# Performance work log

Hardware: AMD Instinct MI355X
Metric: run time of the kernel (lower is better)

## Reference

```python
import jax, jax.numpy as jnp
import numpy as np

N_NODES = 50000
N_EDGES = 1600000
IN_DIM = 128
HID = 64
HEADS = 4
N_GRAPHS = 64
OUT_DIM = 10
NEG_SLOPE = 0.2  # PyG GATConv default leaky_relu slope


def _glorot(key, shape):
    fan_in = shape[0] if len(shape) > 1 else shape[-1]
    return jax.random.normal(key, shape, dtype=jnp.float32) / np.sqrt(fan_in)


def setup_inputs() -> dict:
    key = jax.random.key(0)
    ks = jax.random.split(key, 24)
    imgs = jax.random.normal(ks[0], (N_NODES, IN_DIM), dtype=jnp.float32)
    edge_index = jax.random.randint(ks[1], (2, N_EDGES), 0, N_NODES, dtype=jnp.int32)
    batch = jnp.sort(jax.random.randint(ks[2], (N_NODES,), 0, N_GRAPHS, dtype=jnp.int32))
    HC = HID * HEADS
    inp = {
        'imgs': imgs, 'edge_index': edge_index, 'batch': batch,
        # superpixel aggregator: Linear(input_dim, hidden)
        'W_agg': _glorot(ks[3], (IN_DIM, HID)), 'b_agg': jnp.zeros((HID,), jnp.float32),
        # GAT layer 0: hidden -> heads*hidden, concat
        'W0': _glorot(ks[4], (HID, HC)), 'as0': _glorot(ks[5], (HEADS, HID)), 'ad0': _glorot(ks[6], (HEADS, HID)), 'b0': jnp.zeros((HC,), jnp.float32),
        # GAT layer 1: heads*hidden -> heads*hidden, concat
        'W1': _glorot(ks[7], (HC, HC)), 'as1': _glorot(ks[8], (HEADS, HID)), 'ad1': _glorot(ks[9], (HEADS, HID)), 'b1': jnp.zeros((HC,), jnp.float32),
        # GAT layer 2: heads*hidden -> hidden, mean over heads
        'W2': _glorot(ks[10], (HC, HC)), 'as2': _glorot(ks[11], (HEADS, HID)), 'ad2': _glorot(ks[12], (HEADS, HID)), 'b2': jnp.zeros((HID,), jnp.float32),
        # MLP: hidden -> hidden -> out
        'mW1': _glorot(ks[13], (HID, HID)), 'mb1': jnp.zeros((HID,), jnp.float32),
        'mW2': _glorot(ks[14], (HID, OUT_DIM)), 'mb2': jnp.zeros((OUT_DIM,), jnp.float32),
    }
    return inp


def _gat_conv(x, src, dst, W, a_src, a_dst, b, concat):
    # PyG GATConv: linear -> per-head scores -> leaky_relu -> segment softmax over dst -> scatter-add
    N = x.shape[0]
    H, C = a_src.shape
    h = (x @ W).reshape(N, H, C)                      # [N,H,C]
    es = jnp.sum(h * a_src, axis=-1)                  # [N,H]
    ed = jnp.sum(h * a_dst, axis=-1)                  # [N,H]
    e = jax.nn.leaky_relu(es[src] + ed[dst], NEG_SLOPE)  # [E,H]
    m = jax.ops.segment_max(e, dst, num_segments=N)
    m = jnp.where(jnp.isfinite(m), m, 0.0)
    ex = jnp.exp(e - m[dst])                          # [E,H]
    s = jax.ops.segment_sum(ex, dst, num_segments=N)
    alpha = ex / (s[dst] + 1e-16)                     # [E,H]
    out = jax.ops.segment_sum(h[src] * alpha[..., None], dst, num_segments=N)  # [N,H,C]
    out = out.reshape(N, H * C) if concat else out.mean(axis=1)
    return out + b


def _forward(imgs, edge_index, batch, W_agg, b_agg, W0, as0, ad0, b0, W1, as1, ad1, b1, W2, as2, ad2, b2, mW1, mb1, mW2, mb2):
    N = imgs.shape[0]
    # add self loops (PyG GATConv default add_self_loops=True)
    loop = jnp.arange(N, dtype=edge_index.dtype)
    src = jnp.concatenate([edge_index[0], loop])
    dst = jnp.concatenate([edge_index[1], loop])
    x = imgs @ W_agg + b_agg                          # lrgb aggregator
    x = jax.nn.elu(_gat_conv(x, src, dst, W0, as0, ad0, b0, True))
    x = jax.nn.elu(_gat_conv(x, src, dst, W1, as1, ad1, b1, True))
    x = _gat_conv(x, src, dst, W2, as2, ad2, b2, False)
    # global mean pool over graphs
    sums = jax.ops.segment_sum(x, batch, num_segments=N_GRAPHS)
    cnt = jax.ops.segment_sum(jnp.ones((N,), x.dtype), batch, num_segments=N_GRAPHS)
    pooled = sums / jnp.maximum(cnt, 1.0)[:, None]
    # MLP (dropout inactive at inference)
    hmlp = jax.nn.relu(pooled @ mW1 + mb1)
    return hmlp @ mW2 + mb2


def reference(imgs, edge_index, batch, W_agg, b_agg, W0, as0, ad0, b0, W1, as1, ad1, b1, W2, as2, ad2, b2, mW1, mb1, mW2, mb2):
    return _forward(imgs, edge_index, batch, W_agg, b_agg, W0, as0, ad0, b0, W1, as1, ad1, b1, W2, as2, ad2, b2, mW1, mb1, mW2, mb2)
```

## Files before the change

### kernel.cpp

```cpp
#include <hip/hip_runtime.h>
#include <hip/hip_bf16.h>

#define N_NODES 50000
#define N_EDGESX 1600000
#define E_TOT   (N_EDGESX + N_NODES)
#define IN_DIM 128
#define HID 64
#define HEADS 4
#define HC 256
#define N_GRAPHS 64
#define OUT_DIM 10
#define NEG_SLOPE 0.2f

#define NBUK 196
#define CAP 12288
#define BT 4096

typedef __attribute__((ext_vector_type(8))) short bf16x8;
typedef __attribute__((ext_vector_type(4))) float f32x4;

__device__ __forceinline__ float lrelu(float x){ return fmaxf(x, NEG_SLOPE*x); }
__device__ __forceinline__ float sel4(float4 v, int i){
  float r = v.x;
  r = (i==1) ? v.y : r;
  r = (i==2) ? v.z : r;
  r = (i==3) ? v.w : r;
  return r;
}
__device__ __forceinline__ unsigned short f2bf(float f){
  union { __hip_bfloat16 b; unsigned short u; } cv;
  cv.b = __float2bfloat16(f);
  return cv.u;
}
__device__ __forceinline__ float bflo(unsigned int u){ return __uint_as_float(u << 16); }
__device__ __forceinline__ float bfhi(unsigned int u){ return __uint_as_float(u & 0xffff0000u); }

__global__ __launch_bounds__(256) void bin_k(const int* __restrict__ ei,
                                             int* __restrict__ bucket_cursor,
                                             unsigned int* __restrict__ bucket_buf){
  __shared__ unsigned int pk[BT];
  __shared__ unsigned int binned[BT];
  __shared__ int hist[256], excl[256], gbase[256], lcur[256], tmp[256];
  const int tid = threadIdx.x;
  const int e0 = blockIdx.x * BT;
  const int nv = min(BT, E_TOT - e0);
  hist[tid] = 0;
  __syncthreads();
  for (int i = tid; i < nv; i += 256){
    int e = e0 + i;
    int src, dst;
    if (e < N_EDGESX){ src = ei[e]; dst = ei[N_EDGESX + e]; }
    else { src = e - N_EDGESX; dst = src; }
    pk[i] = ((unsigned)src << 16) | (unsigned)dst;
    atomicAdd(&hist[dst >> 8], 1);
  }
  __syncthreads();
  int v = hist[tid];
  tmp[tid] = v;
  __syncthreads();
  for (int off = 1; off < 256; off <<= 1){
    int t = (tid >= off) ? tmp[tid-off] : 0;
    __syncthreads();
    tmp[tid] += t;
    __syncthreads();
  }
  excl[tid] = tmp[tid] - v;
  lcur[tid] = tmp[tid] - v;
  if (tid < NBUK && v > 0) gbase[tid] = atomicAdd(&bucket_cursor[tid], v);
  __syncthreads();
  for (int i = tid; i < nv; i += 256){
    unsigned u = pk[i];
    int b = (int)((u & 0xFFFFu) >> 8);
    int p = atomicAdd(&lcur[b], 1);
    binned[p] = u;
  }
  __syncthreads();
  for (int j = tid; j < nv; j += 256){
    unsigned u = binned[j];
    int b = (int)((u & 0xFFFFu) >> 8);
    bucket_buf[(size_t)b*CAP + gbase[b] + (j - excl[b])] = u;
  }
}

__global__ __launch_bounds__(256) void bucket_scan_k(const int* __restrict__ bucket_cursor,
                                                     int* __restrict__ bucket_base,
                                                     int* __restrict__ row_start){
  __shared__ int tmp[256];
  int t = threadIdx.x;
  int v = (t < NBUK) ? bucket_cursor[t] : 0;
  tmp[t] = v;
  __syncthreads();
  for (int off = 1; off < 256; off <<= 1){
    int x = (t >= off) ? tmp[t-off] : 0;
    __syncthreads();
    tmp[t] += x;
    __syncthreads();
  }
  if (t < NBUK) bucket_base[t] = tmp[t] - v;
  if (t == 0) row_start[N_NODES] = E_TOT;
}

__global__ __launch_bounds__(256) void build_k(const unsigned int* __restrict__ bucket_buf,
                                               const int* __restrict__ bucket_cursor,
                                               const int* __restrict__ bucket_base,
                                               int* __restrict__ row_start,
                                               int* __restrict__ csr_src){
  __shared__ int hist[256], excl[256], lcur[256], tmp[256];
  const int b = blockIdx.x;
  const int t = threadIdx.x;
  const int cntb = bucket_cursor[b];
  const int base = bucket_base[b];
  const unsigned int* buf = bucket_buf + (size_t)b*CAP;
  hist[t] = 0;
  __syncthreads();
  for (int i = t; i < cntb; i += 256) atomicAdd(&hist[buf[i] & 255], 1);
  __syncthreads();
  int v = hist[t];
  tmp[t] = v;
  __syncthreads();
  for (int off = 1; off < 256; off <<= 1){
    int x = (t >= off) ? tmp[t-off] : 0;
    __syncthreads();
    tmp[t] += x;
    __syncthreads();
  }
  excl[t] = tmp[t] - v;
  lcur[t] = tmp[t] - v;
  int g = b*256 + t;
  if (g < N_NODES) row_start[g] = base + excl[t];
  __syncthreads();
  for (int i = t; i < cntb; i += 256){
    unsigned u = buf[i];
    int p = atomicAdd(&lcur[u & 255], 1);
    csr_src[base + p] = (int)(u >> 16);
  }
}

__global__ __launch_bounds__(256) void wcvt_k(const float* __restrict__ W, unsigned short* __restrict__ WT, int K){
  int idx = blockIdx.x*256 + threadIdx.x;
  if (idx >= K*256) return;
  int k = idx >> 8, c = idx & 255;
  WT[c*K + k] = f2bf(W[k*256 + c]);
}

__global__ __launch_bounds__(256) void wproj_k(const float* __restrict__ W0,
    const float* __restrict__ as0, const float* __restrict__ ad0,
    float* __restrict__ ws0, float* __restrict__ wd0){
  int t = threadIdx.x;
  int h = t >> 6, k = t & 63;
  float s = 0.f, d = 0.f;
  for (int c = 0; c < 64; c++){
    float wv = W0[k*256 + h*64 + c];
    s = fmaf(wv, as0[h*64 + c], s);
    d = fmaf(wv, ad0[h*64 + c], d);
  }
  ws0[t] = s; wd0[t] = d;
}

__global__ __launch_bounds__(256) void agg_lin(const float* __restrict__ imgs, const float* __restrict__ W,
                                               const float* __restrict__ b,
                                               const float* __restrict__ ws0, const float* __restrict__ wd0,
                                               unsigned short* __restrict__ x0,
                                               float* __restrict__ es, float* __restrict__ ed){
  __shared__ __align__(16) float xr[4][IN_DIM];
  int w = threadIdx.x >> 6, lane = threadIdx.x & 63;
  int n = blockIdx.x*4 + w;
  if (n >= N_NODES) return;
  ((float2*)xr[w])[lane] = ((const float2*)(imgs + (size_t)n*IN_DIM))[lane];
  float acc = b[lane];
  #pragma unroll 8
  for (int k = 0; k < IN_DIM; k++)
    acc = fmaf(xr[w][k], W[k*HID + lane], acc);
  x0[(size_t)n*HID + lane] = f2bf(acc);
  float p[4], q[4];
  #pragma unroll
  for (int h = 0; h < 4; h++){
    p[h] = acc * ws0[h*64 + lane];
    q[h] = acc * wd0[h*64 + lane];
  }
  #pragma unroll
  for (int off = 32; off >= 1; off >>= 1){
    #pragma unroll
    for (int h = 0; h < 4; h++){
      p[h] += __shfl_xor(p[h], off);
      q[h] += __shfl_xor(q[h], off);
    }
  }
  if (lane == 0){
    float4 pv; pv.x=p[0]; pv.y=p[1]; pv.z=p[2]; pv.w=p[3];
    float4 qv; qv.x=q[0]; qv.y=q[1]; qv.z=q[2]; qv.w=q[3];
    *(float4*)(es + n*4) = pv;
    *(float4*)(ed + n*4) = qv;
  }
}

__global__ __launch_bounds__(256) void gat_agg0(const unsigned short* __restrict__ x0,
    const float* __restrict__ es, const float* __restrict__ ed,
    const int* __restrict__ row_start, const int* __restrict__ csr_src,
    unsigned short* __restrict__ y4){
  __shared__ int   sbuf[4][64];
  __shared__ float wbuf[4][64][4];
  const int lane = threadIdx.x & 63;
  const int wid  = threadIdx.x >> 6;
  const int n = blockIdx.x*4 + wid;
  if (n >= N_NODES) return;
  const int rs = row_start[n], re = row_start[n+1];
  const float4 edn = *(const float4*)(ed + n*4);
  const int slot = lane >> 3;
  const int f8   = lane & 7;
  float4 sumw = make_float4(0.f,0.f,0.f,0.f);
  float acc[4][8];
  #pragma unroll
  for (int h=0;h<4;h++)
    #pragma unroll
    for (int q2=0;q2<8;q2++) acc[h][q2]=0.f;

  for (int base = rs; base < re; base += 64){
    const int cl = min(64, re - base);
    int e = base + lane;
    int s = (e < re) ? csr_src[e] : 0;
    float4 e4 = *(const float4*)(es + (s<<2));
    float w0 = __expf(lrelu(e4.x + edn.x));
    float w1 = __expf(lrelu(e4.y + edn.y));
    float w2 = __expf(lrelu(e4.z + edn.z));
    float w3 = __expf(lrelu(e4.w + edn.w));
    if (e >= re){ w0=0.f; w1=0.f; w2=0.f; w3=0.f; }
    sumw.x += w0; sumw.y += w1; sumw.z += w2; sumw.w += w3;
    sbuf[wid][lane] = s;
    float4 wv; wv.x=w0; wv.y=w1; wv.z=w2; wv.w=w3;
    *(float4*)wbuf[wid][lane] = wv;
    for (int j = 0; j < cl; j += 8){
      int jj = j + slot;
      if (jj < cl){
        float4 aw = *(const float4*)wbuf[wid][jj];
        int s2 = sbuf[wid][jj];
        uint4 hv = *(const uint4*)(x0 + ((unsigned)(s2<<6) + (unsigned)(f8<<3)));
        float f[8] = {bflo(hv.x),bfhi(hv.x),bflo(hv.y),bfhi(hv.y),
                      bflo(hv.z),bfhi(hv.z),bflo(hv.w),bfhi(hv.w)};
        #pragma unroll
        for (int q2=0;q2<8;q2++){
          acc[0][q2] = fmaf(aw.x, f[q2], acc[0][q2]);
          acc[1][q2] = fmaf(aw.y, f[q2], acc[1][q2]);
          acc[2][q2] = fmaf(aw.z, f[q2], acc[2][q2]);
          acc[3][q2] = fmaf(aw.w, f[q2], acc[3][q2]);
        }
      }
    }
  }
  #pragma unroll
  for (int off = 8; off <= 32; off <<= 1){
    #pragma unroll
    for (int h=0;h<4;h++)
      #pragma unroll
      for (int q2=0;q2<8;q2++) acc[h][q2] += __shfl_xor(acc[h][q2], off);
  }
  #pragma unroll
  for (int off = 32; off >= 1; off >>= 1){
    sumw.x += __shfl_xor(sumw.x, off);
    sumw.y += __shfl_xor(sumw.y, off);
    sumw.z += __shfl_xor(sumw.z, off);
    sumw.w += __shfl_xor(sumw.w, off);
  }
  if (lane < 32){
    int h = lane >> 3;
    float inv = 1.f / (sel4(sumw, h) + 1e-16f);
    union { unsigned short u[8]; uint4 v; } ob;
    #pragma unroll
    for (int q2=0;q2<8;q2++) ob.u[q2] = f2bf(acc[h][q2] * inv);
    *(uint4*)(y4 + (size_t)n*HC + lane*8) = ob.v;
  }
}

__global__ __launch_bounds__(256) void hgemm_k(const unsigned short* __restrict__ y4,
                                               const unsigned short* __restrict__ WT0,
                                               const float* __restrict__ b0,
                                               unsigned short* __restrict__ x1){
  __shared__ __align__(16) unsigned short xs[16][264];
  const int tid = threadIdx.x;
  const int lane = tid & 63;
  const int w = tid >> 6;
  const int n0 = blockIdx.x * 16;
  for (int i = tid; i < 16*32; i += 256){
    int r = i >> 5, cc = (i & 31) * 8;
    *(uint4*)(&xs[r][cc]) = *(const uint4*)(y4 + (size_t)(n0+r)*HC + cc);
  }
  __syncthreads();
  const int g = lane >> 4, cl = lane & 15;
  f32x4 acc[4];
  #pragma unroll
  for (int c = 0; c < 4; c++) acc[c] = (f32x4){0.f,0.f,0.f,0.f};
  #pragma unroll
  for (int t = 0; t < 2; t++){
    bf16x8 a = *(const bf16x8*)(&xs[cl][w*64 + t*32 + g*8]);
    #pragma unroll
    for (int c = 0; c < 4; c++){
      bf16x8 bv = *(const bf16x8*)(WT0 + (size_t)(w*64 + c*16 + cl)*64 + t*32 + g*8);
      acc[c] = __builtin_amdgcn_mfma_f32_16x16x32_bf16(a, bv, acc[c], 0, 0, 0);
    }
  }
  #pragma unroll
  for (int c = 0; c < 4; c++){
    int col = w*64 + c*16 + cl;
    float bb = b0[col];
    #pragma unroll
    for (int j = 0; j < 4; j++){
      float v = acc[c][j] + bb;
      v = v > 0.f ? v : expm1f(v);
      x1[(size_t)(n0 + g*4 + j)*HC + col] = f2bf(v);
    }
  }
}

template<int K>
__global__ __launch_bounds__(256) void lin_mfma(const unsigned short* __restrict__ x,
                                                const unsigned short* __restrict__ WT,
                                                const float* __restrict__ as_, const float* __restrict__ ad_,
                                                unsigned short* __restrict__ h,
                                                float* __restrict__ es, float* __restrict__ ed){
  constexpr int KP = K + 8;
  __shared__ __align__(16) unsigned short xs[16][KP];
  const int tid = threadIdx.x;
  const int lane = tid & 63;
  const int w = tid >> 6;
  const int n0 = blockIdx.x * 16;
  constexpr int CH = K/8;
  for (int i = tid; i < 16*CH; i += 256){
    int r = i / CH, cc = (i % CH)*8;
    *(uint4*)(&xs[r][cc]) = *(const uint4*)(x + (size_t)(n0+r)*K + cc);
  }
  __syncthreads();
  const int g  = lane >> 4;
  const int cl = lane & 15;
  f32x4 acc[4];
  #pragma unroll
  for (int c = 0; c < 4; c++) acc[c] = (f32x4){0.f,0.f,0.f,0.f};
  #pragma unroll
  for (int t = 0; t < K/32; t++){
    bf16x8 a = *(const bf16x8*)(&xs[cl][t*32 + g*8]);
    #pragma unroll
    for (int c = 0; c < 4; c++){
      bf16x8 bv = *(const bf16x8*)(WT + (size_t)(w*64 + c*16 + cl)*K + t*32 + g*8);
      acc[c] = __builtin_amdgcn_mfma_f32_16x16x32_bf16(a, bv, acc[c], 0, 0, 0);
    }
  }
  float pes[4] = {0.f,0.f,0.f,0.f}, ped[4] = {0.f,0.f,0.f,0.f};
  #pragma unroll
  for (int c = 0; c < 4; c++){
    float av = as_[w*64 + c*16 + cl];
    float dv = ad_[w*64 + c*16 + cl];
    #pragma unroll
    for (int j = 0; j < 4; j++){
      pes[j] = fmaf(acc[c][j], av, pes[j]);
      ped[j] = fmaf(acc[c][j], dv, ped[j]);
    }
  }
  #pragma unroll
  for (int off = 8; off >= 1; off >>= 1){
    #pragma unroll
    for (int j = 0; j < 4; j++){
      pes[j] += __shfl_xor(pes[j], off);
      ped[j] += __shfl_xor(ped[j], off);
    }
  }
  if (cl == 0){
    #pragma unroll
    for (int j = 0; j < 4; j++){
      int n = n0 + g*4 + j;
      es[n*4 + w] = pes[j];
      ed[n*4 + w] = ped[j];
    }
  }
  #pragma unroll
  for (int c = 0; c < 4; c++){
    #pragma unroll
    for (int j = 0; j < 4; j++){
      h[(size_t)(n0 + g*4 + j)*HC + w*64 + c*16 + cl] = f2bf(acc[c][j]);
    }
  }
}

template<int ACT, int OBF>
__global__ __launch_bounds__(256) void gat_agg(const unsigned short* __restrict__ h,
    const float* __restrict__ es, const float* __restrict__ ed,
    const int* __restrict__ row_start, const int* __restrict__ csr_src,
    const float* __restrict__ bias, void* __restrict__ outp){
  __shared__ int   sbuf[4][64];
  __shared__ float wbuf[4][64][4];
  const int lane = threadIdx.x & 63;
  const int wid  = threadIdx.x >> 6;
  const int n = blockIdx.x*4 + wid;
  if (n >= N_NODES) return;
  const int rs = row_start[n], re = row_start[n+1];
  const float4 edn = *(const float4*)(ed + n*4);
  const int half = lane >> 5;
  const int l5   = lane & 31;
  const int hh   = l5 >> 3;
  const unsigned voff_lane = (unsigned)(l5 << 3);

  float4 sum4 = make_float4(0.f,0.f,0.f,0.f);
  float a0=0.f,a1=0.f,a2=0.f,a3=0.f,a4=0.f,a5=0.f,a6=0.f,a7=0.f;

  for (int base = rs; base < re; base += 64){
    const int cl = min(64, re - base);
    int e = base + lane;
    int s = (e < re) ? csr_src[e] : 0;
    float4 e4 = *(const float4*)(es + (s<<2));
    float w0 = __expf(lrelu(e4.x + edn.x));
    float w1 = __expf(lrelu(e4.y + edn.y));
    float w2 = __expf(lrelu(e4.z + edn.z));
    float w3 = __expf(lrelu(e4.w + edn.w));
    if (e >= re){ w0=0.f; w1=0.f; w2=0.f; w3=0.f; }
    sum4.x += w0; sum4.y += w1; sum4.z += w2; sum4.w += w3;
    sbuf[wid][lane] = s;
    float4 wv4; wv4.x=w0; wv4.y=w1; wv4.z=w2; wv4.w=w3;
    *(float4*)wbuf[wid][lane] = wv4;
    for (int j = 0; j < cl; j += 2){
      int jj = j + half;
      float a  = wbuf[wid][jj][hh];
      int   s2 = sbuf[wid][jj];
      uint4 hv = *(const uint4*)(h + ((unsigned)(s2<<8) + voff_lane));
      a0 = fmaf(a, bflo(hv.x), a0);
      a1 = fmaf(a, bfhi(hv.x), a1);
      a2 = fmaf(a, bflo(hv.y), a2);
      a3 = fmaf(a, bfhi(hv.y), a3);
      a4 = fmaf(a, bflo(hv.z), a4);
      a5 = fmaf(a, bfhi(hv.z), a5);
      a6 = fmaf(a, bflo(hv.w), a6);
      a7 = fmaf(a, bfhi(hv.w), a7);
    }
  }
  #pragma unroll
  for (int off = 32; off >= 1; off >>= 1){
    sum4.x += __shfl_xor(sum4.x, off);
    sum4.y += __shfl_xor(sum4.y, off);
    sum4.z += __shfl_xor(sum4.z, off);
    sum4.w += __shfl_xor(sum4.w, off);
  }
  const float inv = 1.f / (sel4(sum4, hh) + 1e-16f);
  a0 += __shfl_xor(a0, 32); a1 += __shfl_xor(a1, 32);
  a2 += __shfl_xor(a2, 32); a3 += __shfl_xor(a3, 32);
  a4 += __shfl_xor(a4, 32); a5 += __shfl_xor(a5, 32);
  a6 += __shfl_xor(a6, 32); a7 += __shfl_xor(a7, 32);
  float4 o;
  o.x = (half ? a4 : a0) * inv;
  o.y = (half ? a5 : a1) * inv;
  o.z = (half ? a6 : a2) * inv;
  o.w = (half ? a7 : a3) * inv;
  const int fbase = l5*8 + half*4;
  if (ACT){
    float4 b4 = *(const float4*)(bias + fbase);
    o.x += b4.x; o.y += b4.y; o.z += b4.z; o.w += b4.w;
    o.x = o.x > 0.f ? o.x : expm1f(o.x);
    o.y = o.y > 0.f ? o.y : expm1f(o.y);
    o.z = o.z > 0.f ? o.z : expm1f(o.z);
    o.w = o.w > 0.f ? o.w : expm1f(o.w);
  }
  if (OBF){
    ushort4 ob;
    ob.x = f2bf(o.x); ob.y = f2bf(o.y); ob.z = f2bf(o.z); ob.w = f2bf(o.w);
    *(ushort4*)((unsigned short*)outp + (size_t)n*HC + fbase) = ob;
  } else {
    *(float4*)((float*)outp + (size_t)n*HC + fbase) = o;
  }
}

#define PB_NODES 128
__global__ __launch_bounds__(256) void pool_k(const float* __restrict__ xagg,
                                              const int* __restrict__ batch, float* __restrict__ pooled,
                                              float* __restrict__ cnt){
  int c = threadIdx.x & 63;
  int sub = threadIdx.x >> 6;
  int n0 = blockIdx.x * PB_NODES;
  int nend = n0 + PB_NODES; if (nend > N_NODES) nend = N_NODES;
  float acc = 0.f; int curg = -1; int cl = 0;
  for (int n = n0 + sub; n < nend; n += 4){
    int g = batch[n];
    if (g != curg){
      if (curg >= 0){
        unsafeAtomicAdd(pooled + curg*HID + c, acc);
        if (c == 0) unsafeAtomicAdd(cnt + curg, (float)cl);
      }
      curg = g; acc = 0.f; cl = 0;
    }
    const float* r = xagg + (size_t)n*HC;
    acc += 0.25f*(r[c] + r[64+c] + r[128+c] + r[192+c]);
    cl++;
  }
  if (curg >= 0){
    unsafeAtomicAdd(pooled + curg*HID + c, acc);
    if (c == 0) unsafeAtomicAdd(cnt + curg, (float)cl);
  }
}

__global__ __launch_bounds__(64) void mlp_k(const float* __restrict__ pooled, const float* __restrict__ cnt,
                                            const float* __restrict__ b2,
                                            const float* __restrict__ mW1, const float* __restrict__ mb1,
                                            const float* __restrict__ mW2, const float* __restrict__ mb2,
                                            float* __restrict__ out){
  __shared__ float p[HID], h1[HID];
  int g = blockIdx.x, j = threadIdx.x;
  float c = fmaxf(cnt[g], 1.f);
  p[j] = pooled[g*HID + j] / c + b2[j];
  __syncthreads();
  float acc = mb1[j];
  #pragma unroll 8
  for (int k = 0; k < HID; k++) acc = fmaf(p[k], mW1[k*HID + j], acc);
  h1[j] = fmaxf(acc, 0.f);
  __syncthreads();
  if (j < OUT_DIM){
    float a2 = mb2[j];
    #pragma unroll 8
    for (int k = 0; k < HID; k++) a2 = fmaf(h1[k], mW2[k*OUT_DIM + j], a2);
    out[g*OUT_DIM + j] = a2;
  }
}

extern "C" void kernel_launch(void* const* d_in, const int* in_sizes, int n_in,
                              void* d_out, int out_size, void* d_ws, size_t ws_size,
                              hipStream_t stream){
  const float* imgs  = (const float*)d_in[0];
  const int*   ei    = (const int*)d_in[1];
  const int*   batch = (const int*)d_in[2];
  const float* W_agg = (const float*)d_in[3];
  const float* b_agg = (const float*)d_in[4];
  const float* W0 = (const float*)d_in[5];
  const float* as0 = (const float*)d_in[6];
  const float* ad0 = (const float*)d_in[7];
  const float* b0 = (const float*)d_in[8];
  const float* W1 = (const float*)d_in[9];
  const float* as1 = (const float*)d_in[10];
  const float* ad1 = (const float*)d_in[11];
  const float* b1 = (const float*)d_in[12];
  const float* W2 = (const float*)d_in[13];
  const float* as2 = (const float*)d_in[14];
  const float* ad2 = (const float*)d_in[15];
  const float* b2 = (const float*)d_in[16];
  const float* mW1 = (const float*)d_in[17];
  const float* mb1 = (const float*)d_in[18];
  const float* mW2 = (const float*)d_in[19];
  const float* mb2 = (const float*)d_in[20];
  float* out = (float*)d_out;

  float* xf32 = (float*)d_ws;
  unsigned short* y4 = (unsigned short*)xf32;
  unsigned short* hb  = (unsigned short*)(xf32 + (size_t)N_NODES*HC);
  unsigned short* xbf = hb + (size_t)N_NODES*HC;
  float* es   = (float*)(xbf + (size_t)N_NODES*HC);
  float* ed   = es + (size_t)N_NODES*HEADS;
  float* pooled = ed + (size_t)N_NODES*HEADS;
  float* cnt  = pooled + N_GRAPHS*HID;
  float* ws0  = cnt + N_GRAPHS;
  float* wd0  = ws0 + 256;
  int* row_start = (int*)(wd0 + 256);
  int* csr_src   = row_start + (N_NODES+1);
  int* bucket_cursor = csr_src + E_TOT;
  int* bucket_base   = bucket_cursor + NBUK;
  unsigned short* WT0 = (unsigned short*)(bucket_base + NBUK);
  unsigned short* WT1 = WT0 + 256*64;
  unsigned short* WT2 = WT1 + 256*256;
  unsigned int* bucket_buf = (unsigned int*)(WT2 + 256*256);
  unsigned short* x0bf = (unsigned short*)bucket_buf;

  hipMemsetAsync(bucket_cursor, 0, NBUK*sizeof(int), stream);
  bin_k<<<(E_TOT + BT - 1)/BT, 256, 0, stream>>>(ei, bucket_cursor, bucket_buf);
  bucket_scan_k<<<1, 256, 0, stream>>>(bucket_cursor, bucket_base, row_start);
  build_k<<<NBUK, 256, 0, stream>>>(bucket_buf, bucket_cursor, bucket_base, row_start, csr_src);

  wcvt_k<<<(64*256+255)/256, 256, 0, stream>>>(W0, WT0, 64);
  wcvt_k<<<(256*256+255)/256, 256, 0, stream>>>(W1, WT1, 256);
  wcvt_k<<<(256*256+255)/256, 256, 0, stream>>>(W2, WT2, 256);
  wproj_k<<<1, 256, 0, stream>>>(W0, as0, ad0, ws0, wd0);

  const int MB = N_NODES/16;
  const int GB = (N_NODES + 3)/4;

  agg_lin<<<GB, 256, 0, stream>>>(imgs, W_agg, b_agg, ws0, wd0, x0bf, es, ed);

  gat_agg0<<<GB, 256, 0, stream>>>(x0bf, es, ed, row_start, csr_src, y4);
  hgemm_k<<<MB, 256, 0, stream>>>(y4, WT0, b0, xbf);

  lin_mfma<256><<<MB, 256, 0, stream>>>(xbf, WT1, as1, ad1, hb, es, ed);
  gat_agg<1,1><<<GB, 256, 0, stream>>>(hb, es, ed, row_start, csr_src, b1, xbf);

  lin_mfma<256><<<MB, 256, 0, stream>>>(xbf, WT2, as2, ad2, hb, es, ed);
  gat_agg<0,0><<<GB, 256, 0, stream>>>(hb, es, ed, row_start, csr_src, nullptr, xf32);

  hipMemsetAsync(pooled, 0, (N_GRAPHS*HID + N_GRAPHS)*sizeof(float), stream);
  pool_k<<<(N_NODES + PB_NODES - 1)/PB_NODES, 256, 0, stream>>>(xf32, batch, pooled, cnt);
  mlp_k<<<N_GRAPHS, 64, 0, stream>>>(pooled, cnt, b2, mW1, mb1, mW2, mb2, out);
}
```

Baseline: 612.5 us.

## Fuse layer-0 GEMM with layer-1 linear, unroll gathers, store final output in bf16

Merges the layer-0 output GEMM (bias plus ELU) and the layer-1 linear projection with its attention scores into one kernel. The intermediate x1 stays in shared memory instead of being written to global memory and read back. The edge-gather loops in gat_agg0 and gat_agg are unrolled two-way so two independent neighbor loads are in flight per iteration. The last aggregation now writes bf16 instead of fp32, which halves the traffic into the pooling kernel at some cost in precision.

```diff
diff --git a/kernel.cpp b/kernel.cpp
--- a/kernel.cpp
+++ b/kernel.cpp
@@ -32,6 +32,7 @@
   cv.b = __float2bfloat16(f);
   return cv.u;
 }
+__device__ __forceinline__ float bf2f(unsigned short u){ return __uint_as_float(((unsigned)u) << 16); }
 __device__ __forceinline__ float bflo(unsigned int u){ return __uint_as_float(u << 16); }
 __device__ __forceinline__ float bfhi(unsigned int u){ return __uint_as_float(u & 0xffff0000u); }
 
@@ -229,7 +230,33 @@
     sbuf[wid][lane] = s;
     float4 wv; wv.x=w0; wv.y=w1; wv.z=w2; wv.w=w3;
     *(float4*)wbuf[wid][lane] = wv;
-    for (int j = 0; j < cl; j += 8){
+    int j = 0;
+    for (; j + 16 <= cl; j += 16){
+      int j0 = j + slot, j1 = j + 8 + slot;
+      float4 awA = *(const float4*)wbuf[wid][j0]; int sA = sbuf[wid][j0];
+      float4 awB = *(const float4*)wbuf[wid][j1]; int sB = sbuf[wid][j1];
+      uint4 hvA = *(const uint4*)(x0 + ((unsigned)(sA<<6) + (unsigned)(f8<<3)));
+      uint4 hvB = *(const uint4*)(x0 + ((unsigned)(sB<<6) + (unsigned)(f8<<3)));
+      float fA[8] = {bflo(hvA.x),bfhi(hvA.x),bflo(hvA.y),bfhi(hvA.y),
+                     bflo(hvA.z),bfhi(hvA.z),bflo(hvA.w),bfhi(hvA.w)};
+      float fB[8] = {bflo(hvB.x),bfhi(hvB.x),bflo(hvB.y),bfhi(hvB.y),
+                     bflo(hvB.z),bfhi(hvB.z),bflo(hvB.w),bfhi(hvB.w)};
+      #pragma unroll
+      for (int q2=0;q2<8;q2++){
+        acc[0][q2] = fmaf(awA.x, fA[q2], acc[0][q2]);
+        acc[1][q2] = fmaf(awA.y, fA[q2], acc[1][q2]);
+        acc[2][q2] = fmaf(awA.z, fA[q2], acc[2][q2]);
+        acc[3][q2] = fmaf(awA.w, fA[q2], acc[3][q2]);
+      }
+      #pragma unroll
+      for (int q2=0;q2<8;q2++){
+        acc[0][q2] = fmaf(awB.x, fB[q2], acc[0][q2]);
+        acc[1][q2] = fmaf(awB.y, fB[q2], acc[1][q2]);
+        acc[2][q2] = fmaf(awB.z, fB[q2], acc[2][q2]);
+        acc[3][q2] = fmaf(awB.w, fB[q2], acc[3][q2]);
+      }
+    }
+    for (; j < cl; j += 8){
       int jj = j + slot;
       if (jj < cl){
         float4 aw = *(const float4*)wbuf[wid][jj];
@@ -271,11 +298,15 @@
   }
 }
 
-__global__ __launch_bounds__(256) void hgemm_k(const unsigned short* __restrict__ y4,
+__global__ __launch_bounds__(256) void hfuse_k(const unsigned short* __restrict__ y4,
                                                const unsigned short* __restrict__ WT0,
                                                const float* __restrict__ b0,
-                                               unsigned short* __restrict__ x1){
+                                               const unsigned short* __restrict__ WT1,
+                                               const float* __restrict__ as_, const float* __restrict__ ad_,
+                                               unsigned short* __restrict__ h,
+                                               float* __restrict__ es, float* __restrict__ ed){
   __shared__ __align__(16) unsigned short xs[16][264];
+  __shared__ __align__(16) unsigned short x1s[16][264];
   const int tid = threadIdx.x;
   const int lane = tid & 63;
   const int w = tid >> 6;
@@ -286,27 +317,76 @@
   }
   __syncthreads();
   const int g = lane >> 4, cl = lane & 15;
+  {
+    f32x4 acc[4];
+    #pragma unroll
+    for (int c = 0; c < 4; c++) acc[c] = (f32x4){0.f,0.f,0.f,0.f};
+    #pragma unroll
+    for (int t = 0; t < 2; t++){
+      bf16x8 a = *(const bf16x8*)(&xs[cl][w*64 + t*32 + g*8]);
+      #pragma unroll
+      for (int c = 0; c < 4; c++){
+        bf16x8 bv = *(const bf16x8*)(WT0 + (size_t)(w*64 + c*16 + cl)*64 + t*32 + g*8);
+        acc[c] = __builtin_amdgcn_mfma_f32_16x16x32_bf16(a, bv, acc[c], 0, 0, 0);
+      }
+    }
+    #pragma unroll
+    for (int c = 0; c < 4; c++){
+      int col = w*64 + c*16 + cl;
+      float bb = b0[col];
+      #pragma unroll
+      for (int j = 0; j < 4; j++){
+        float v = acc[c][j] + bb;
+        v = v > 0.f ? v : expm1f(v);
+        x1s[g*4 + j][col] = f2bf(v);
+      }
+    }
+  }
+  __syncthreads();
   f32x4 acc[4];
   #pragma unroll
   for (int c = 0; c < 4; c++) acc[c] = (f32x4){0.f,0.f,0.f,0.f};
   #pragma unroll
-  for (int t = 0; t < 2; t++){
-    bf16x8 a = *(const bf16x8*)(&xs[cl][w*64 + t*32 + g*8]);
+  for (int t = 0; t < 8; t++){
+    bf16x8 a = *(const bf16x8*)(&x1s[cl][t*32 + g*8]);
     #pragma unroll
     for (int c = 0; c < 4; c++){
-      bf16x8 bv = *(const bf16x8*)(WT0 + (size_t)(w*64 + c*16 + cl)*64 + t*32 + g*8);
+      bf16x8 bv = *(const bf16x8*)(WT1 + (size_t)(w*64 + c*16 + cl)*HC + t*32 + g*8);
       acc[c] = __builtin_amdgcn_mfma_f32_16x16x32_bf16(a, bv, acc[c], 0, 0, 0);
     }
   }
+  float pes[4] = {0.f,0.f,0.f,0.f}, ped[4] = {0.f,0.f,0.f,0.f};
   #pragma unroll
   for (int c = 0; c < 4; c++){
-    int col = w*64 + c*16 + cl;
-    float bb = b0[col];
-    #pragma unroll
-    for (int j = 0; j < 4; j++){
-      float v = acc[c][j] + bb;
-      v = v > 0.f ? v : expm1f(v);
-      x1[(size_t)(n0 + g*4 + j)*HC + col] = f2bf(v);
+    float av = as_[w*64 + c*16 + cl];
+    float dv = ad_[w*64 + c*16 + cl];
+    #pragma unroll
+    for (int j = 0; j < 4; j++){
+      pes[j] = fmaf(acc[c][j], av, pes[j]);
+      ped[j] = fmaf(acc[c][j], dv, ped[j]);
+    }
+  }
+  #pragma unroll
+  for (int off = 8; off >= 1; off >>= 1){
+    #pragma unroll
+    for (int j = 0; j < 4; j++){
+      pes[j] += __shfl_xor(pes[j], off);
+      ped[j] += __shfl_xor(ped[j], off);
+    }
+  }
+  if (cl == 0){
+    #pragma unroll
+    for (int j = 0; j < 4; j++){
+      int n = n0 + g*4 + j;
+      es[n*4 + w] = pes[j];
+      ed[n*4 + w] = ped[j];
+    }
+  }
+  #pragma unroll
+  for (int c = 0; c < 4; c++){
+    #pragma unroll
+    for (int j = 0; j < 4; j++){
+      h[(size_t)(n0 + g*4 + j)*HC + w*64 + c*16 + cl] = f2bf(acc[c][j]);
     }
   }
 }
@@ -379,11 +459,11 @@
   }
 }
 
-template<int ACT, int OBF>
+template<int ACT>
 __global__ __launch_bounds__(256) void gat_agg(const unsigned short* __restrict__ h,
     const float* __restrict__ es, const float* __restrict__ ed,
     const int* __restrict__ row_start, const int* __restrict__ csr_src,
-    const float* __restrict__ bias, void* __restrict__ outp){
+    const float* __restrict__ bias, unsigned short* __restrict__ outp){
   __shared__ int   sbuf[4][64];
   __shared__ float wbuf[4][64][4];
   const int lane = threadIdx.x & 63;
@@ -414,7 +494,31 @@
     sbuf[wid][lane] = s;
     float4 wv4; wv4.x=w0; wv4.y=w1; wv4.z=w2; wv4.w=w3;
     *(float4*)wbuf[wid][lane] = wv4;
-    for (int j = 0; j < cl; j += 2){
+    int j = 0;
+    for (; j + 4 <= cl; j += 4){
+      int j0 = j + half, j1 = j + 2 + half;
+      float aA = wbuf[wid][j0][hh]; int sA = sbuf[wid][j0];
+      float aB = wbuf[wid][j1][hh]; int sB = sbuf[wid][j1];
+      uint4 hA = *(const uint4*)(h + ((unsigned)(sA<<8) + voff_lane));
+      uint4 hB = *(const uint4*)(h + ((unsigned)(sB<<8) + voff_lane));
+      a0 = fmaf(aA, bflo(hA.x), a0);
+      a1 = fmaf(aA, bfhi(hA.x), a1);
+      a2 = fmaf(aA, bflo(hA.y), a2);
+      a3 = fmaf(aA, bfhi(hA.y), a3);
+      a4 = fmaf(aA, bflo(hA.z), a4);
+      a5 = fmaf(aA, bfhi(hA.z), a5);
+      a6 = fmaf(aA, bflo(hA.w), a6);
+      a7 = fmaf(aA, bfhi(hA.w), a7);
+      a0 = fmaf(aB, bflo(hB.x), a0);
+      a1 = fmaf(aB, bfhi(hB.x), a1);
+      a2 = fmaf(aB, bflo(hB.y), a2);
+      a3 = fmaf(aB, bfhi(hB.y), a3);
+      a4 = fmaf(aB, bflo(hB.z), a4);
+      a5 = fmaf(aB, bfhi(hB.z), a5);
+      a6 = fmaf(aB, bflo(hB.w), a6);
+      a7 = fmaf(aB, bfhi(hB.w), a7);
+    }
+    for (; j < cl; j += 2){
       int jj = j + half;
       float a  = wbuf[wid][jj][hh];
       int   s2 = sbuf[wid][jj];
@@ -455,17 +559,13 @@
     o.z = o.z > 0.f ? o.z : expm1f(o.z);
     o.w = o.w > 0.f ? o.w : expm1f(o.w);
   }
-  if (OBF){
-    ushort4 ob;
-    ob.x = f2bf(o.x); ob.y = f2bf(o.y); ob.z = f2bf(o.z); ob.w = f2bf(o.w);
-    *(ushort4*)((unsigned short*)outp + (size_t)n*HC + fbase) = ob;
-  } else {
-    *(float4*)((float*)outp + (size_t)n*HC + fbase) = o;
-  }
+  ushort4 ob;
+  ob.x = f2bf(o.x); ob.y = f2bf(o.y); ob.z = f2bf(o.z); ob.w = f2bf(o.w);
+  *(ushort4*)(outp + (size_t)n*HC + fbase) = ob;
 }
 
 #define PB_NODES 128
-__global__ __launch_bounds__(256) void pool_k(const float* __restrict__ xagg,
+__global__ __launch_bounds__(256) void pool_k(const unsigned short* __restrict__ xagg,
                                               const int* __restrict__ batch, float* __restrict__ pooled,
                                               float* __restrict__ cnt){
   int c = threadIdx.x & 63;
@@ -482,8 +582,8 @@
       }
       curg = g; acc = 0.f; cl = 0;
     }
-    const float* r = xagg + (size_t)n*HC;
-    acc += 0.25f*(r[c] + r[64+c] + r[128+c] + r[192+c]);
+    const unsigned short* r = xagg + (size_t)n*HC;
+    acc += 0.25f*(bf2f(r[c]) + bf2f(r[64+c]) + bf2f(r[128+c]) + bf2f(r[192+c]));
     cl++;
   }
   if (curg >= 0){
@@ -541,9 +641,8 @@
   const float* mb2 = (const float*)d_in[20];
   float* out = (float*)d_out;
 
-  float* xf32 = (float*)d_ws;
-  unsigned short* y4 = (unsigned short*)xf32;
-  unsigned short* hb  = (unsigned short*)(xf32 + (size_t)N_NODES*HC);
+  unsigned short* y4  = (unsigned short*)d_ws;
+  unsigned short* hb  = y4 + (size_t)N_NODES*HC;
   unsigned short* xbf = hb + (size_t)N_NODES*HC;
   float* es   = (float*)(xbf + (size_t)N_NODES*HC);
   float* ed   = es + (size_t)N_NODES*HEADS;
@@ -577,15 +676,14 @@
   agg_lin<<<GB, 256, 0, stream>>>(imgs, W_agg, b_agg, ws0, wd0, x0bf, es, ed);
 
   gat_agg0<<<GB, 256, 0, stream>>>(x0bf, es, ed, row_start, csr_src, y4);
-  hgemm_k<<<MB, 256, 0, stream>>>(y4, WT0, b0, xbf);
-
-  lin_mfma<256><<<MB, 256, 0, stream>>>(xbf, WT1, as1, ad1, hb, es, ed);
-  gat_agg<1,1><<<GB, 256, 0, stream>>>(hb, es, ed, row_start, csr_src, b1, xbf);
+
+  hfuse_k<<<MB, 256, 0, stream>>>(y4, WT0, b0, WT1, as1, ad1, hb, es, ed);
+  gat_agg<1><<<GB, 256, 0, stream>>>(hb, es, ed, row_start, csr_src, b1, xbf);
 
   lin_mfma<256><<<MB, 256, 0, stream>>>(xbf, WT2, as2, ad2, hb, es, ed);
-  gat_agg<0,0><<<GB, 256, 0, stream>>>(hb, es, ed, row_start, csr_src, nullptr, xf32);
+  gat_agg<0><<<GB, 256, 0, stream>>>(hb, es, ed, row_start, csr_src, nullptr, xbf);
 
   hipMemsetAsync(pooled, 0, (N_GRAPHS*HID + N_GRAPHS)*sizeof(float), stream);
-  pool_k<<<(N_NODES + PB_NODES - 1)/PB_NODES, 256, 0, stream>>>(xf32, batch, pooled, cnt);
+  pool_k<<<(N_NODES + PB_NODES - 1)/PB_NODES, 256, 0, stream>>>(xbf, batch, pooled, cnt);
   mlp_k<<<N_GRAPHS, 64, 0, stream>>>(pooled, cnt, b2, mW1, mb1, mW2, mb2, out);
 }
```

New measurement: 591.2 us. 1.04x faster.
